# Performance work log

Measured on AMD Instinct MI355X. Metric: run time of the kernel, lower is better.

## Reference

```python
import jax, jax.numpy as jnp
import numpy as np
import math

N_HEADS = 4
IN_DIM = 1024
DIM_HEAD = IN_DIM // N_HEADS


def setup_inputs() -> dict:
    key = jax.random.key(0)
    ks = jax.random.split(key, 5)
    x = jax.random.normal(ks[0], (8, 2048, IN_DIM), dtype=jnp.float32)
    std = 0.02
    W_Q = jax.random.normal(ks[1], (N_HEADS, IN_DIM, DIM_HEAD), dtype=jnp.float32) * std
    W_K = jax.random.normal(ks[2], (N_HEADS, IN_DIM, DIM_HEAD), dtype=jnp.float32) * std
    W_V = jax.random.normal(ks[3], (N_HEADS, IN_DIM, DIM_HEAD), dtype=jnp.float32) * std
    W_O = jax.random.normal(ks[4], (N_HEADS, DIM_HEAD, IN_DIM), dtype=jnp.float32) * std
    b_Q = jnp.zeros((N_HEADS, DIM_HEAD), dtype=jnp.float32)
    b_K = jnp.zeros((N_HEADS, DIM_HEAD), dtype=jnp.float32)
    b_V = jnp.zeros((N_HEADS, DIM_HEAD), dtype=jnp.float32)
    b_O = jnp.zeros((IN_DIM,), dtype=jnp.float32)
    return {"normalized_resid_pre": x, "W_Q": W_Q, "b_Q": b_Q, "W_K": W_K,
            "b_K": b_K, "W_V": W_V, "b_V": b_V, "W_O": W_O, "b_O": b_O}


def reference(normalized_resid_pre, W_Q, b_Q, W_K, b_K, W_V, b_V, W_O, b_O):
    x = normalized_resid_pre  # [n, s, d_model]
    # projections: [n, s, h, dh]
    q = jnp.einsum('nsd,hde->nshe', x, W_Q) + b_Q
    k = jnp.einsum('nsd,hde->nshe', x, W_K) + b_K
    v = jnp.einsum('nsd,hde->nshe', x, W_V) + b_V
    scale = 1.0 / math.sqrt(DIM_HEAD)
    scores = jnp.einsum('nqhe,nkhe->nhqk', q, k) * scale  # [n, h, q, k]
    pattern = jax.nn.softmax(scores, axis=-1)
    z = jnp.einsum('nhqk,nkhe->nqhe', pattern, v)  # [n, q, h, dh]
    out = jnp.einsum('nqhe,hed->nqd', z, W_O) + b_O  # [n, q, d_model]
    return out
```

## Files before the change

kernel.cpp:

```cpp
#include <hip/hip_runtime.h>

typedef __attribute__((ext_vector_type(8))) short short8;
typedef __attribute__((ext_vector_type(4))) float floatx4;
typedef __attribute__((ext_vector_type(16))) float floatx16;
typedef __attribute__((ext_vector_type(4))) unsigned short ushort4v;
typedef __attribute__((ext_vector_type(2))) unsigned int uint2v;
typedef unsigned short u16;

__device__ __forceinline__ u16 f2bf(float f) {
  unsigned u = __float_as_uint(f);
  u += 0x7fffu + ((u >> 16) & 1u);
  return (u16)(u >> 16);
}

__device__ __forceinline__ void gl_lds16(const void* g, void* l) {
  __builtin_amdgcn_global_load_lds((const __attribute__((address_space(1))) void*)g,
                                   (__attribute__((address_space(3))) void*)l, 16, 0, 0);
}

__device__ __forceinline__ float bpermf(float v, int srclane) {
  return __int_as_float(__builtin_amdgcn_ds_bpermute(srclane << 2, __float_as_int(v)));
}


__global__ void k_cvt_x(const float* __restrict__ x, u16* __restrict__ o, long n) {
  long i = ((long)blockIdx.x * blockDim.x + threadIdx.x) * 8;
  long stride = (long)gridDim.x * blockDim.x * 8;
  for (; i < n; i += stride) {
    float4 a = *(const float4*)(x + i);
    float4 b = *(const float4*)(x + i + 4);
    ushort4v r0 = { f2bf(a.x), f2bf(a.y), f2bf(a.z), f2bf(a.w) };
    ushort4v r1 = { f2bf(b.x), f2bf(b.y), f2bf(b.z), f2bf(b.w) };
    *(ushort4v*)(o + i) = r0;
    *(ushort4v*)(o + i + 4) = r1;
  }
}

__global__ __launch_bounds__(256) void k_cvt_w(
    const float* __restrict__ WQ, const float* __restrict__ WK,
    const float* __restrict__ WV, const float* __restrict__ WO,
    u16* __restrict__ wqkv, u16* __restrict__ wo) {
  __shared__ float tile[64][65];
  const int bid = blockIdx.x;
  const float* src;
  u16* dst;
  int C, R, r0, c0;
  if (bid < 768) {
    int th = bid >> 6;
    int tid6 = bid & 63;
    int t = th >> 2, h = th & 3;
    src = ((t == 0) ? WQ : (t == 1) ? WK : WV) + h * 1024 * 256;
    dst = wqkv + (size_t)(t * 1024 + h * 256) * 1024;
    R = 1024; C = 256;
    r0 = (tid6 & 15) * 64;
    c0 = (tid6 >> 4) * 64;
  } else {
    int tid6 = bid - 768;
    src = WO; dst = wo;
    R = 1024; C = 1024;
    r0 = (tid6 & 15) * 64;
    c0 = (tid6 >> 4) * 64;
  }
  const int tx = threadIdx.x & 15, ty = threadIdx.x >> 4;
#pragma unroll
  for (int i = 0; i < 4; ++i) {
    int r = ty + 16 * i;
    float4 v = *(const float4*)(src + (long)(r0 + r) * C + c0 + tx * 4);
    tile[r][tx * 4 + 0] = v.x;
    tile[r][tx * 4 + 1] = v.y;
    tile[r][tx * 4 + 2] = v.z;
    tile[r][tx * 4 + 3] = v.w;
  }
  __syncthreads();
#pragma unroll
  for (int i = 0; i < 4; ++i) {
    int c = ty + 16 * i;
    ushort4v o = { f2bf(tile[tx * 4 + 0][c]), f2bf(tile[tx * 4 + 1][c]),
                   f2bf(tile[tx * 4 + 2][c]), f2bf(tile[tx * 4 + 3][c]) };
    *(ushort4v*)(dst + (long)(c0 + c) * R + r0 + tx * 4) = o;
  }
}

template<int EPI>
__global__ __launch_bounds__(256, 2) void k_gemm(
    const u16* __restrict__ A, const u16* __restrict__ Bt,
    u16* __restrict__ Qo, u16* __restrict__ Ko, u16* __restrict__ Vt,
    const float* __restrict__ bQ, const float* __restrict__ bK, const float* __restrict__ bV,
    float* __restrict__ out, const float* __restrict__ bO) {
  __shared__ u16 sA[128 * 64];
  __shared__ u16 sB[128 * 64];
  const int tid = threadIdx.x;
  const int lane = tid & 63, w = tid >> 6;
  const int wr = w >> 1, wc = w & 1;
  const int cI = lane & 15, rI = lane >> 4;
  const long am0 = (long)blockIdx.y * 128;
  const long bn0 = (long)blockIdx.x * 128;
  floatx4 acc[4][4] = {};

  for (int kt = 0; kt < 1024; kt += 64) {
#pragma unroll
    for (int j = 0; j < 4; ++j) {
      int o = j * 4096 + w * 1024 + lane * 16;
      int row = o >> 7, c = (o & 127) >> 1;
      gl_lds16(A + (am0 + row) * 1024 + kt + c, (char*)sA + o);
      gl_lds16(Bt + (bn0 + row) * 1024 + kt + c, (char*)sB + o);
    }
    __syncthreads();
#pragma unroll
    for (int kk = 0; kk < 2; ++kk) {
      short8 af[4], bf[4];
      const int ko = kk * 64 + rI * 16;
#pragma unroll
      for (int i = 0; i < 4; ++i) {
        af[i] = *(const short8*)((const char*)sA + (wr * 64 + i * 16 + cI) * 128 + ko);
        bf[i] = *(const short8*)((const char*)sB + (wc * 64 + i * 16 + cI) * 128 + ko);
      }
#pragma unroll
      for (int i = 0; i < 4; ++i)
#pragma unroll
        for (int jn = 0; jn < 4; ++jn)
          acc[i][jn] = __builtin_amdgcn_mfma_f32_16x16x32_bf16(af[i], bf[jn], acc[i][jn], 0, 0, 0);
    }
    __syncthreads();
  }

  if (EPI == 0) {
    const int t = (int)(bn0 >> 10);
    const float* bias = (t == 0) ? bQ : (t == 1) ? bK : bV;
    const float sc = (t == 0) ? 0.0625f * 1.44269504088896f : 1.0f;
#pragma unroll
    for (int i = 0; i < 4; ++i) {
      int m = (int)am0 + wr * 64 + i * 16 + rI * 4;
      int b = m >> 11, s = m & 2047;
#pragma unroll
      for (int jn = 0; jn < 4; ++jn) {
        int n = (int)bn0 + wc * 64 + jn * 16 + cI;
        int h = (n >> 8) & 3, e = n & 255;
        float bb = bias[n & 1023];
        floatx4 c = acc[i][jn];
        if (t < 2) {
          u16* dst = (t == 0) ? Qo : Ko;
          long base = ((long)(b * 4 + h) * 2048 + s) * 256 + e;
          dst[base]       = f2bf((c[0] + bb) * sc);
          dst[base + 256] = f2bf((c[1] + bb) * sc);
          dst[base + 512] = f2bf((c[2] + bb) * sc);
          dst[base + 768] = f2bf((c[3] + bb) * sc);
        } else {
          long base = ((long)(b * 4 + h) * 256 + e) * 2048 + s;
          ushort4v v = { f2bf(c[0] + bb), f2bf(c[1] + bb), f2bf(c[2] + bb), f2bf(c[3] + bb) };
          *(ushort4v*)(Vt + base) = v;
        }
      }
    }
  } else {
#pragma unroll
    for (int i = 0; i < 4; ++i) {
      int m = (int)am0 + wr * 64 + i * 16 + rI * 4;
#pragma unroll
      for (int jn = 0; jn < 4; ++jn) {
        int n = (int)bn0 + wc * 64 + jn * 16 + cI;
        float bb = bO[n];
        floatx4 c = acc[i][jn];
        out[(long)m * 1024 + n]       = c[0] + bb;
        out[(long)(m + 1) * 1024 + n] = c[1] + bb;
        out[(long)(m + 2) * 1024 + n] = c[2] + bb;
        out[(long)(m + 3) * 1024 + n] = c[3] + bb;
      }
    }
  }
}

__global__ __launch_bounds__(256, 2) void k_attn(
    const u16* __restrict__ Q, const u16* __restrict__ K,
    const u16* __restrict__ Vt, u16* __restrict__ Z) {
  extern __shared__ u16 smem[];
  u16* sK = smem;
  u16* sV = smem + 16384;
  const int tid = threadIdx.x, lane = tid & 63, w = tid >> 6;
  const int q = lane & 31, hi = lane >> 5;
  const int role = (blockIdx.x & 7) * 64 + (blockIdx.x >> 3);
  const int bh = role >> 4, qt = role & 15;
  const long base = (long)bh * 2048 * 256;
  const int q0 = qt * 128 + w * 32;

  int off_ds[4], ksrc[4], vsrc[4];
#pragma unroll
  for (int j = 0; j < 4; ++j) {
    int o = j * 4096 + tid * 16;
    off_ds[j] = o;
    int krow = o >> 9, kch = (o >> 4) & 31;
    ksrc[j] = krow * 256 + ((kch ^ (krow & 7)) << 3);
    int e = o >> 6, cr = (o >> 4) & 3;
    vsrc[j] = e * 2048 + ((cr ^ ((e >> 1) & 3)) << 3);
  }
  const u16* Kg0 = K + base;
  const u16* Vg  = Vt + base;

  short8 qf[16];
#pragma unroll
  for (int ec = 0; ec < 16; ++ec)
    qf[ec] = *(const short8*)(Q + base + (long)(q0 + q) * 256 + ec * 16 + hi * 8);

#define STAGE_K(kt_, buf_) do { \
    const u16* Kg_ = Kg0 + (kt_) * 8192; \
    u16* dK_ = sK + (buf_) * 8192; \
    _Pragma("unroll") \
    for (int j = 0; j < 4; ++j) gl_lds16(Kg_ + ksrc[j], (char*)dK_ + off_ds[j]); \
  } while (0)
#define STAGE_V(kt_, buf_) do { \
    const u16* Vg_ = Vg + (kt_) * 32; \
    u16* dV_ = sV + (buf_) * 8192; \
    _Pragma("unroll") \
    for (int j = 0; j < 4; ++j) gl_lds16(Vg_ + vsrc[j], (char*)dV_ + off_ds[j]); \
  } while (0)

  STAGE_K(0, 0);

  floatx16 z[8] = {};
  float m_run = -1e30f, l = 0.f;
  const int ksw = q & 7, vsw = (q >> 1) & 3;
  short8 pa0 = {}, pa1 = {};

  __syncthreads();

  for (int t = 0; t < 64; ++t) {
    const int cb = t & 1;
    if (t < 63) STAGE_K(t + 1, cb ^ 1);
    STAGE_V(t, cb);
    const char* pK = (const char*)(sK + cb * 8192);
    const char* pV = (const char*)(sV + (cb ^ 1) * 8192);

    floatx16 s = {};
    __builtin_amdgcn_s_setprio(1);
    if (t > 0) {
#pragma unroll
      for (int u = 0; u < 8; ++u) {
        short8 kf0 = *(const short8*)(pK + (q << 9) + ((((4 * u) | hi) ^ ksw) << 4));
        s = __builtin_amdgcn_mfma_f32_32x32x16_bf16(kf0, qf[2 * u], s, 0, 0, 0);
        short8 vf0 = *(const short8*)(pV + ((u * 32 + q) << 6) + (((hi ^ vsw) & 3) << 4));
        z[u] = __builtin_amdgcn_mfma_f32_32x32x16_bf16(pa0, vf0, z[u], 0, 0, 0);
        short8 kf1 = *(const short8*)(pK + (q << 9) + ((((4 * u + 2) | hi) ^ ksw) << 4));
        s = __builtin_amdgcn_mfma_f32_32x32x16_bf16(kf1, qf[2 * u + 1], s, 0, 0, 0);
        short8 vf1 = *(const short8*)(pV + ((u * 32 + q) << 6) + ((((2 | hi) ^ vsw) & 3) << 4));
        z[u] = __builtin_amdgcn_mfma_f32_32x32x16_bf16(pa1, vf1, z[u], 0, 0, 0);
      }
    } else {
#pragma unroll
      for (int ec = 0; ec < 16; ++ec) {
        short8 kf = *(const short8*)(pK + (q << 9) + ((((2 * ec) | hi) ^ ksw) << 4));
        s = __builtin_amdgcn_mfma_f32_32x32x16_bf16(kf, qf[ec], s, 0, 0, 0);
      }
    }
    __builtin_amdgcn_s_setprio(0);

    float m0 = fmaxf(s[0], s[1]),  m1 = fmaxf(s[2], s[3]);
    float m2 = fmaxf(s[4], s[5]),  m3 = fmaxf(s[6], s[7]);
    float m4 = fmaxf(s[8], s[9]),  m5 = fmaxf(s[10], s[11]);
    float m6 = fmaxf(s[12], s[13]), m7 = fmaxf(s[14], s[15]);
    m0 = fmaxf(m0, m1); m2 = fmaxf(m2, m3); m4 = fmaxf(m4, m5); m6 = fmaxf(m6, m7);
    m0 = fmaxf(m0, m2); m4 = fmaxf(m4, m6);
    float pm = fmaxf(m0, m4);
    {
      uint2v sw = __builtin_amdgcn_permlane32_swap(__float_as_uint(pm), __float_as_uint(pm), false, false);
      pm = fmaxf(__uint_as_float(sw[0]), __uint_as_float(sw[1]));
    }

    if (!__all(pm <= m_run + 8.f)) {
      float mn = fmaxf(m_run, pm);
      float esc = exp2f(m_run - mn);
      l *= esc;
      m_run = mn;
      float escv[16];
#pragma unroll
      for (int r = 0; r < 16; ++r)
        escv[r] = bpermf(esc, ((r & 3) + 8 * (r >> 2) + 4 * hi) + 32 * hi);
#pragma unroll
      for (int et = 0; et < 8; ++et)
#pragma unroll
        for (int r = 0; r < 16; ++r) z[et][r] *= escv[r];
    }

    float p[16], rs = 0.f;
#pragma unroll
    for (int r = 0; r < 16; ++r) { p[r] = exp2f(s[r] - m_run); rs += p[r]; }
    {
      uint2v sw = __builtin_amdgcn_permlane32_swap(__float_as_uint(rs), __float_as_uint(rs), false, false);
      l += __uint_as_float(sw[0]) + __uint_as_float(sw[1]);
    }

    unsigned w0, w1, w2, w3, w4, w5, w6, w7;
    asm("v_cvt_pk_bf16_f32 %0, %1, %2" : "=v"(w0) : "v"(p[0]), "v"(p[1]));
    asm("v_cvt_pk_bf16_f32 %0, %1, %2" : "=v"(w1) : "v"(p[2]), "v"(p[3]));
    asm("v_cvt_pk_bf16_f32 %0, %1, %2" : "=v"(w2) : "v"(p[4]), "v"(p[5]));
    asm("v_cvt_pk_bf16_f32 %0, %1, %2" : "=v"(w3) : "v"(p[6]), "v"(p[7]));
    asm("v_cvt_pk_bf16_f32 %0, %1, %2" : "=v"(w4) : "v"(p[8]), "v"(p[9]));
    asm("v_cvt_pk_bf16_f32 %0, %1, %2" : "=v"(w5) : "v"(p[10]), "v"(p[11]));
    asm("v_cvt_pk_bf16_f32 %0, %1, %2" : "=v"(w6) : "v"(p[12]), "v"(p[13]));
    asm("v_cvt_pk_bf16_f32 %0, %1, %2" : "=v"(w7) : "v"(p[14]), "v"(p[15]));
    uint2v e02 = __builtin_amdgcn_permlane32_swap(w0, w2, false, false);
    uint2v e13 = __builtin_amdgcn_permlane32_swap(w1, w3, false, false);
    uint2v e46 = __builtin_amdgcn_permlane32_swap(w4, w6, false, false);
    uint2v e57 = __builtin_amdgcn_permlane32_swap(w5, w7, false, false);
    int4 t0i = { (int)e02[0], (int)e13[0], (int)e02[1], (int)e13[1] };
    int4 t1i = { (int)e46[0], (int)e57[0], (int)e46[1], (int)e57[1] };
    pa0 = *(short8*)&t0i;
    pa1 = *(short8*)&t1i;

    __syncthreads();
  }

  {
    const char* pV = (const char*)(sV + 8192);
#pragma unroll
    for (int u = 0; u < 8; ++u) {
      short8 vf0 = *(const short8*)(pV + ((u * 32 + q) << 6) + (((hi ^ vsw) & 3) << 4));
      z[u] = __builtin_amdgcn_mfma_f32_32x32x16_bf16(pa0, vf0, z[u], 0, 0, 0);
      short8 vf1 = *(const short8*)(pV + ((u * 32 + q) << 6) + ((((2 | hi) ^ vsw) & 3) << 4));
      z[u] = __builtin_amdgcn_mfma_f32_32x32x16_bf16(pa1, vf1, z[u], 0, 0, 0);
    }
  }

  float linv = 1.f / l;
  float invv[16];
#pragma unroll
  for (int r = 0; r < 16; ++r)
    invv[r] = bpermf(linv, ((r & 3) + 8 * (r >> 2) + 4 * hi) + 32 * hi);

  const int b = bh >> 2, hh = bh & 3;
  const long zb = (long)b * 2048 * 1024 + hh * 256;
#pragma unroll
  for (int r = 0; r < 16; ++r) {
    const int qr = (r & 3) + 8 * (r >> 2) + 4 * hi;
    long rb = zb + (long)(q0 + qr) * 1024;
#pragma unroll
    for (int et = 0; et < 8; ++et)
      Z[rb + et * 32 + q] = f2bf(z[et][r] * invv[r]);
  }
#undef STAGE_K
#undef STAGE_V
}


extern "C" void kernel_launch(void* const* d_in, const int* in_sizes, int n_in,
                              void* d_out, int out_size, void* d_ws, size_t ws_size,
                              hipStream_t stream) {
  const float* x  = (const float*)d_in[0];
  const float* WQ = (const float*)d_in[1];
  const float* bQ = (const float*)d_in[2];
  const float* WK = (const float*)d_in[3];
  const float* bK = (const float*)d_in[4];
  const float* WV = (const float*)d_in[5];
  const float* bV = (const float*)d_in[6];
  const float* WO = (const float*)d_in[7];
  const float* bO = (const float*)d_in[8];
  float* out = (float*)d_out;

  char* p = (char*)d_ws;
  u16* xb   = (u16*)p; p += (size_t)16384 * 1024 * 2;
  u16* wqkv = (u16*)p; p += (size_t)3072 * 1024 * 2;
  u16* wo   = (u16*)p; p += (size_t)1024 * 1024 * 2;
  u16* Qb   = (u16*)p; p += (size_t)32 * 2048 * 256 * 2;
  u16* Kb   = (u16*)p; p += (size_t)32 * 2048 * 256 * 2;
  u16* Vtb  = (u16*)p; p += (size_t)32 * 256 * 2048 * 2;
  u16* Zb   = xb;

  const int attn_lds = 65536;
  (void)hipFuncSetAttribute((const void*)k_attn,
                            hipFuncAttributeMaxDynamicSharedMemorySize, attn_lds);

  k_cvt_x<<<dim3(4096), dim3(256), 0, stream>>>(x, xb, (long)16384 * 1024);
  k_cvt_w<<<dim3(1024), dim3(256), 0, stream>>>(WQ, WK, WV, WO, wqkv, wo);
  k_gemm<0><<<dim3(24, 128), dim3(256), 0, stream>>>(xb, wqkv, Qb, Kb, Vtb, bQ, bK, bV,
                                                     (float*)nullptr, (const float*)nullptr);
  k_attn<<<dim3(512), dim3(256), attn_lds, stream>>>(Qb, Kb, Vtb, Zb);
  k_gemm<1><<<dim3(8, 128), dim3(256), 0, stream>>>(Zb, wo,
                                                    (u16*)nullptr, (u16*)nullptr, (u16*)nullptr,
                                                    (const float*)nullptr, (const float*)nullptr, (const float*)nullptr,
                                                    out, bO);
}
```

Baseline: 391.9 us.

## Rewrite projection GEMMs as 256x256 tiled 8-wave pipelined kernel with swizzled LDS

Replaces the 128x128 single-buffered GEMM with a 512-thread kernel that computes 256x256 tiles. It double-buffers K tiles in 128KB of dynamic LDS using global_load_lds, XOR-swizzles the LDS layout to avoid bank conflicts, and interleaves staged loads with MFMA phases using explicit waitcnt, barriers and setprio. It also remaps block IDs for L2 locality. This is meant to raise data reuse per tile and hide global-load latency, at the cost of one workgroup per CU on LDS, heavy register use for 32 accumulators, and fragile hand-written synchronisation.

Measured after the change: 360.0 us. 1.09x faster.

```diff
diff --git a/kernel.cpp b/kernel.cpp
--- a/kernel.cpp
+++ b/kernel.cpp
@@ -21,6 +21,8 @@
 __device__ __forceinline__ float bpermf(float v, int srclane) {
   return __int_as_float(__builtin_amdgcn_ds_bpermute(srclane << 2, __float_as_int(v)));
 }
+
+#define BARRIER() do { asm volatile("" ::: "memory"); __builtin_amdgcn_s_barrier(); asm volatile("" ::: "memory"); } while (0)
 
 
 __global__ void k_cvt_x(const float* __restrict__ x, u16* __restrict__ o, long n) {
@@ -82,62 +84,120 @@
 }
 
 template<int EPI>
-__global__ __launch_bounds__(256, 2) void k_gemm(
+__global__ __launch_bounds__(512, 2) void k_gemm8(
     const u16* __restrict__ A, const u16* __restrict__ Bt,
     u16* __restrict__ Qo, u16* __restrict__ Ko, u16* __restrict__ Vt,
     const float* __restrict__ bQ, const float* __restrict__ bK, const float* __restrict__ bV,
-    float* __restrict__ out, const float* __restrict__ bO) {
-  __shared__ u16 sA[128 * 64];
-  __shared__ u16 sB[128 * 64];
-  const int tid = threadIdx.x;
-  const int lane = tid & 63, w = tid >> 6;
-  const int wr = w >> 1, wc = w & 1;
+    float* __restrict__ out, const float* __restrict__ bO, int gridNx) {
+  extern __shared__ char lds[];
+  const int tid = threadIdx.x, lane = tid & 63, w = tid >> 6;
+  const int wm = w >> 2, wn = w & 3;
   const int cI = lane & 15, rI = lane >> 4;
-  const long am0 = (long)blockIdx.y * 128;
-  const long bn0 = (long)blockIdx.x * 128;
-  floatx4 acc[4][4] = {};
-
-  for (int kt = 0; kt < 1024; kt += 64) {
-#pragma unroll
-    for (int j = 0; j < 4; ++j) {
-      int o = j * 4096 + w * 1024 + lane * 16;
-      int row = o >> 7, c = (o & 127) >> 1;
-      gl_lds16(A + (am0 + row) * 1024 + kt + c, (char*)sA + o);
-      gl_lds16(Bt + (bn0 + row) * 1024 + kt + c, (char*)sB + o);
-    }
-    __syncthreads();
-#pragma unroll
-    for (int kk = 0; kk < 2; ++kk) {
-      short8 af[4], bf[4];
-      const int ko = kk * 64 + rI * 16;
-#pragma unroll
-      for (int i = 0; i < 4; ++i) {
-        af[i] = *(const short8*)((const char*)sA + (wr * 64 + i * 16 + cI) * 128 + ko);
-        bf[i] = *(const short8*)((const char*)sB + (wc * 64 + i * 16 + cI) * 128 + ko);
-      }
-#pragma unroll
-      for (int i = 0; i < 4; ++i)
-#pragma unroll
-        for (int jn = 0; jn < 4; ++jn)
-          acc[i][jn] = __builtin_amdgcn_mfma_f32_16x16x32_bf16(af[i], bf[jn], acc[i][jn], 0, 0, 0);
-    }
-    __syncthreads();
+  const int nwg = gridDim.x;
+  const int bid = blockIdx.x;
+  const int swz = (bid & 7) * (nwg >> 3) + (bid >> 3);
+  const int by = swz / gridNx, bx = swz % gridNx;
+  const long am0 = (long)by * 256, bn0 = (long)bx * 256;
+
+  int so_ds[2], so_src[2];
+#pragma unroll
+  for (int jj = 0; jj < 2; ++jj) {
+    int o = jj * 8192 + tid * 16;
+    int row = o >> 7;
+    so_ds[jj] = o;
+    so_src[jj] = row * 1024 + ((((o >> 4) & 7) ^ (row & 7)) << 3);
+  }
+  const u16* gAlo = A + am0 * 1024;
+  const u16* gAhi = gAlo + 128 * 1024;
+  const u16* gBlo = Bt + bn0 * 1024;
+  const u16* gBhi = gBlo + 128 * 1024;
+
+#define STG(gp, kt, ldsbyte) do { \
+    gl_lds16((gp) + (kt) * 64 + so_src[0], lds + (ldsbyte) + so_ds[0]); \
+    gl_lds16((gp) + (kt) * 64 + so_src[1], lds + (ldsbyte) + so_ds[1]); \
+  } while (0)
+
+  floatx4 acc[8][4] = {};
+
+  STG(gAlo, 0, 0);
+  STG(gBlo, 0, 65536);
+  STG(gAhi, 0, 16384);
+  STG(gBhi, 0, 81920);
+  STG(gAlo, 1, 32768);
+  STG(gBlo, 1, 98304);
+  asm volatile("s_waitcnt vmcnt(4)" ::: "memory");
+  BARRIER();
+
+#define PHASE(AB, BB, MH, NH, STAGE_STMT, VMSTMT) do { \
+    short8 af[4][2], bf[2][2]; \
+    _Pragma("unroll") \
+    for (int mi2 = 0; mi2 < 4; ++mi2) { \
+      int row = wm * 64 + mi2 * 16 + cI; \
+      const char* rp = lds + (AB) + (MH) * 16384 + row * 128; \
+      int sw = row & 7; \
+      _Pragma("unroll") \
+      for (int kk = 0; kk < 2; ++kk) \
+        af[mi2][kk] = *(const short8*)(rp + (((kk * 4 + rI) ^ sw) << 4)); \
+    } \
+    _Pragma("unroll") \
+    for (int ni2 = 0; ni2 < 2; ++ni2) { \
+      int row = wn * 32 + ni2 * 16 + cI; \
+      const char* rp = lds + (BB) + (NH) * 16384 + row * 128; \
+      int sw = row & 7; \
+      _Pragma("unroll") \
+      for (int kk = 0; kk < 2; ++kk) \
+        bf[ni2][kk] = *(const short8*)(rp + (((kk * 4 + rI) ^ sw) << 4)); \
+    } \
+    STAGE_STMT; \
+    VMSTMT; \
+    BARRIER(); \
+    __builtin_amdgcn_s_setprio(1); \
+    _Pragma("unroll") \
+    for (int mi2 = 0; mi2 < 4; ++mi2) \
+      _Pragma("unroll") \
+      for (int ni2 = 0; ni2 < 2; ++ni2) \
+        _Pragma("unroll") \
+        for (int kk = 0; kk < 2; ++kk) \
+          acc[(MH) * 4 + mi2][(NH) * 2 + ni2] = __builtin_amdgcn_mfma_f32_16x16x32_bf16( \
+              af[mi2][kk], bf[ni2][kk], acc[(MH) * 4 + mi2][(NH) * 2 + ni2], 0, 0, 0); \
+    __builtin_amdgcn_s_setprio(0); \
+    BARRIER(); \
+  } while (0)
+
+  for (int it = 0; it < 8; ++it) {
+    const int u = 2 * it;
+    const bool s2 = (u + 2 < 16), s3 = (u + 3 < 16);
+    PHASE(0, 65536, 0, 0, STG(gAhi, u + 1, 49152), );
+    PHASE(0, 65536, 0, 1, STG(gBhi, u + 1, 114688), );
+    PHASE(0, 65536, 1, 0, if (s2) STG(gAlo, u + 2, 0), );
+    PHASE(0, 65536, 1, 1, if (s2) STG(gBlo, u + 2, 65536),
+          if (s2) { asm volatile("s_waitcnt vmcnt(4)" ::: "memory"); }
+          else    { asm volatile("s_waitcnt vmcnt(0)" ::: "memory"); });
+    PHASE(32768, 98304, 0, 0, if (s2) STG(gAhi, u + 2, 16384), );
+    PHASE(32768, 98304, 0, 1, if (s2) STG(gBhi, u + 2, 81920), );
+    PHASE(32768, 98304, 1, 0, if (s3) STG(gAlo, u + 3, 32768), );
+    PHASE(32768, 98304, 1, 1, if (s3) STG(gBlo, u + 3, 98304),
+          asm volatile("s_waitcnt vmcnt(4)" ::: "memory"));
   }
 
   if (EPI == 0) {
     const int t = (int)(bn0 >> 10);
+    const int h = (int)(bn0 >> 8) & 3;
     const float* bias = (t == 0) ? bQ : (t == 1) ? bK : bV;
     const float sc = (t == 0) ? 0.0625f * 1.44269504088896f : 1.0f;
 #pragma unroll
-    for (int i = 0; i < 4; ++i) {
-      int m = (int)am0 + wr * 64 + i * 16 + rI * 4;
+    for (int MH = 0; MH < 2; ++MH)
+#pragma unroll
+    for (int mi = 0; mi < 4; ++mi) {
+      int m = (int)am0 + MH * 128 + wm * 64 + mi * 16 + rI * 4;
       int b = m >> 11, s = m & 2047;
 #pragma unroll
-      for (int jn = 0; jn < 4; ++jn) {
-        int n = (int)bn0 + wc * 64 + jn * 16 + cI;
-        int h = (n >> 8) & 3, e = n & 255;
-        float bb = bias[n & 1023];
-        floatx4 c = acc[i][jn];
+      for (int NH = 0; NH < 2; ++NH)
+#pragma unroll
+      for (int ni = 0; ni < 2; ++ni) {
+        int e = NH * 128 + wn * 32 + ni * 16 + cI;
+        float bb = bias[h * 256 + e];
+        floatx4 c = acc[MH * 4 + mi][NH * 2 + ni];
         if (t < 2) {
           u16* dst = (t == 0) ? Qo : Ko;
           long base = ((long)(b * 4 + h) * 2048 + s) * 256 + e;
@@ -154,13 +214,17 @@
     }
   } else {
 #pragma unroll
-    for (int i = 0; i < 4; ++i) {
-      int m = (int)am0 + wr * 64 + i * 16 + rI * 4;
-#pragma unroll
-      for (int jn = 0; jn < 4; ++jn) {
-        int n = (int)bn0 + wc * 64 + jn * 16 + cI;
+    for (int MH = 0; MH < 2; ++MH)
+#pragma unroll
+    for (int mi = 0; mi < 4; ++mi) {
+      int m = (int)am0 + MH * 128 + wm * 64 + mi * 16 + rI * 4;
+#pragma unroll
+      for (int NH = 0; NH < 2; ++NH)
+#pragma unroll
+      for (int ni = 0; ni < 2; ++ni) {
+        int n = (int)bn0 + NH * 128 + wn * 32 + ni * 16 + cI;
         float bb = bO[n];
-        floatx4 c = acc[i][jn];
+        floatx4 c = acc[MH * 4 + mi][NH * 2 + ni];
         out[(long)m * 1024 + n]       = c[0] + bb;
         out[(long)(m + 1) * 1024 + n] = c[1] + bb;
         out[(long)(m + 2) * 1024 + n] = c[2] + bb;
@@ -168,6 +232,8 @@
       }
     }
   }
+#undef PHASE
+#undef STG
 }
 
 __global__ __launch_bounds__(256, 2) void k_attn(
@@ -367,14 +433,19 @@
   const int attn_lds = 65536;
   (void)hipFuncSetAttribute((const void*)k_attn,
                             hipFuncAttributeMaxDynamicSharedMemorySize, attn_lds);
+  const int gemm_lds = 131072;
+  (void)hipFuncSetAttribute((const void*)k_gemm8<0>,
+                            hipFuncAttributeMaxDynamicSharedMemorySize, gemm_lds);
+  (void)hipFuncSetAttribute((const void*)k_gemm8<1>,
+                            hipFuncAttributeMaxDynamicSharedMemorySize, gemm_lds);
 
   k_cvt_x<<<dim3(4096), dim3(256), 0, stream>>>(x, xb, (long)16384 * 1024);
   k_cvt_w<<<dim3(1024), dim3(256), 0, stream>>>(WQ, WK, WV, WO, wqkv, wo);
-  k_gemm<0><<<dim3(24, 128), dim3(256), 0, stream>>>(xb, wqkv, Qb, Kb, Vtb, bQ, bK, bV,
-                                                     (float*)nullptr, (const float*)nullptr);
+  k_gemm8<0><<<dim3(768), dim3(512), gemm_lds, stream>>>(xb, wqkv, Qb, Kb, Vtb, bQ, bK, bV,
+                                                         (float*)nullptr, (const float*)nullptr, 12);
   k_attn<<<dim3(512), dim3(256), attn_lds, stream>>>(Qb, Kb, Vtb, Zb);
-  k_gemm<1><<<dim3(8, 128), dim3(256), 0, stream>>>(Zb, wo,
-                                                    (u16*)nullptr, (u16*)nullptr, (u16*)nullptr,
-                                                    (const float*)nullptr, (const float*)nullptr, (const float*)nullptr,
-                                                    out, bO);
-}
+  k_gemm8<1><<<dim3(256), dim3(512), gemm_lds, stream>>>(Zb, wo,
+                                                         (u16*)nullptr, (u16*)nullptr, (u16*)nullptr,
+                                                         (const float*)nullptr, (const float*)nullptr, (const float*)nullptr,
+                                                         out, bO, 4);
+}
```
